# Kernel tuning notes

Measured on AMD Instinct MI355X. Metric: run time of the kernel, lower is better.

Reference implementation:

```python
import jax, jax.numpy as jnp
import numpy as np

B, S, H = 4, 2048, 768
NUM_HEADS = 12
HEAD_DIM = H // NUM_HEADS


def setup_inputs() -> dict:
    key = jax.random.key(0)
    k1, k2, k3 = jax.random.split(key, 3)
    hidden_states = jax.random.normal(k1, (B, S, H), dtype=jnp.float32)
    # torch Linear weight [out,in]; store transposed [in,out] for x @ W
    w_qkv = jax.random.normal(k2, (H, 3 * H), dtype=jnp.float32) * (1.0 / np.sqrt(H))
    w_out = jax.random.normal(k3, (H, H), dtype=jnp.float32) * (1.0 / np.sqrt(H))
    return {"hidden_states": hidden_states, "w_qkv": w_qkv, "w_out": w_out}


def reference(hidden_states, w_qkv, w_out):
    b, s, h = hidden_states.shape
    qkv = hidden_states @ w_qkv                      # [b,s,3h]
    qkv = qkv.reshape(b, s, 3, NUM_HEADS, HEAD_DIM)
    qkv = jnp.transpose(qkv, (2, 0, 3, 1, 4))        # [3,b,nh,s,hd]
    q, k, v = qkv[0], qkv[1], qkv[2]
    scale = 1.0 / np.sqrt(HEAD_DIM).astype(np.float32)
    scores = jnp.einsum('bhqd,bhkd->bhqk', q, k) * scale   # [b,nh,s,s]
    causal = jnp.triu(jnp.ones((s, s), dtype=bool), k=1)
    scores = jnp.where(causal, jnp.float32(-jnp.inf), scores)
    attn = jax.nn.softmax(scores, axis=-1)
    # dropout is identity in eval mode
    out = jnp.einsum('bhqk,bhkd->bhqd', attn, v)      # [b,nh,s,hd]
    out = jnp.transpose(out, (0, 2, 1, 3)).reshape(b, s, h)
    return out @ w_out
```

## Files before the change

### kernel.cpp

```cpp
#include <hip/hip_runtime.h>
#include <stdint.h>

#define B_ 4
#define S_ 2048
#define H_ 768
#define NH_ 12
#define HD_ 64
#define BH_ (B_ * NH_)

#define QSCALE 0.18033688011112042f

typedef __attribute__((ext_vector_type(4))) float f32x4;
typedef __attribute__((ext_vector_type(16))) float f32x16;
typedef __attribute__((ext_vector_type(8))) __bf16 bf16x8;
typedef __attribute__((ext_vector_type(8))) unsigned short ushort8;
typedef __attribute__((ext_vector_type(2))) unsigned int u32x2;
typedef __attribute__((ext_vector_type(4))) unsigned int u32x4;

__device__ __forceinline__ unsigned short bf16rne(float f) {
  union { float f; unsigned int u; } v;
  v.f = f;
  unsigned int u = v.u;
  return (unsigned short)((u + 0x7fffu + ((u >> 16) & 1u)) >> 16);
}

#if __has_builtin(__builtin_amdgcn_cvt_pk_bf16_f32)
__device__ __forceinline__ unsigned int pk2(float a, float b) {
  auto r = __builtin_amdgcn_cvt_pk_bf16_f32(a, b);
  return *(unsigned int*)&r;
}
#else
__device__ __forceinline__ unsigned int pk2(float a, float b) {
  return (unsigned int)bf16rne(a) | ((unsigned int)bf16rne(b) << 16);
}
#endif

#if __has_builtin(__builtin_amdgcn_exp2f)
#define EXP2F(x) __builtin_amdgcn_exp2f(x)
#else
#define EXP2F(x) exp2f(x)
#endif

#if __has_builtin(__builtin_amdgcn_permlane32_swap)
__device__ __forceinline__ u32x2 permswap(unsigned a, unsigned b) {
  u32x2 r = __builtin_amdgcn_permlane32_swap(a, b, false, false);
  return r;
}
#else
__device__ __forceinline__ u32x2 permswap(unsigned a, unsigned b) {
  int l = (int)(threadIdx.x & 63);
  unsigned ap = (unsigned)__shfl((int)a, l ^ 32, 64);
  unsigned bp = (unsigned)__shfl((int)b, l ^ 32, 64);
  u32x2 r;
  r[0] = (l & 32) ? bp : a;
  r[1] = (l & 32) ? b : ap;
  return r;
}
#endif

__device__ __forceinline__ void gll16(const void* g, void* l) {
  __builtin_amdgcn_global_load_lds(
      (const __attribute__((address_space(1))) unsigned int*)g,
      (__attribute__((address_space(3))) unsigned int*)l, 16, 0, 0);
}

__device__ __forceinline__ void tconv_body(const float* __restrict__ in,
                                           unsigned short* __restrict__ out,
                                           int R, int C, int bx, int by,
                                           unsigned short (*tile)[72], int tid) {
  int c0 = bx * 64, r0 = by * 64;
#pragma unroll
  for (int i = 0; i < 4; ++i) {
    int c = i * 256 + tid;
    int row = c >> 4, col4 = (c & 15) * 4;
    float4 v = *(const float4*)(in + (size_t)(r0 + row) * C + c0 + col4);
    *(uint2*)(&tile[row][col4]) = (uint2){pk2(v.x, v.y), pk2(v.z, v.w)};
  }
  __syncthreads();
#pragma unroll
  for (int i = 0; i < 2; ++i) {
    int c = i * 256 + tid;
    int oc = c >> 3, r8 = (c & 7) * 8;
    ushort8 v;
#pragma unroll
    for (int j = 0; j < 8; ++j) v[j] = tile[r8 + j][oc];
    *(ushort8*)(out + (size_t)(c0 + oc) * R + r0 + r8) = v;
  }
}

__global__ __launch_bounds__(256) void prep_kernel(const float* __restrict__ hs,
                                                   const float* __restrict__ wqkv,
                                                   const float* __restrict__ wout,
                                                   unsigned short* __restrict__ Xbf,
                                                   unsigned short* __restrict__ Wqkvt,
                                                   unsigned short* __restrict__ Woutt) {
  __shared__ unsigned short tile[64][72];
  int bid = blockIdx.x, tid = threadIdx.x;
  if (bid < 3072) {
    int i = (bid * 256 + tid) * 8;
    const float4* p = (const float4*)(hs + i);
    float4 a = p[0], b = p[1];
    uint4 r = {pk2(a.x, a.y), pk2(a.z, a.w), pk2(b.x, b.y), pk2(b.z, b.w)};
    *(uint4*)(Xbf + i) = r;
  } else if (bid < 3504) {
    int idx = bid - 3072;
    tconv_body(wqkv, Wqkvt, 768, 2304, idx % 36, idx / 36, tile, tid);
  } else {
    int idx = bid - 3504;
    tconv_body(wout, Woutt, 768, 768, idx % 12, idx / 12, tile, tid);
  }
}

template <int MODE>
__device__ __forceinline__ void gemm_core(const unsigned short* __restrict__ A,
                                          const unsigned short* __restrict__ Bm,
                                          void* __restrict__ Cout, int N, int K,
                                          int bm, int bn,
                                          unsigned short* As, unsigned short* Bs) {
  int tid = threadIdx.x;
  int lane = tid & 63, wave = tid >> 6;
  int quad = lane >> 4, l16 = lane & 15;
  int wm = (wave & 1) * 64, wn = (wave >> 1) * 64;
  const unsigned short* Ag = A + (size_t)bm * 128 * K;
  const unsigned short* Bg = Bm + (size_t)bn * 128 * K;

  f32x4 zero = {0.f, 0.f, 0.f, 0.f};
  f32x4 acc[4][4];
#pragma unroll
  for (int mt = 0; mt < 4; ++mt)
#pragma unroll
    for (int nt = 0; nt < 4; ++nt) acc[mt][nt] = zero;

  for (int k0 = 0; k0 < K; k0 += 32) {
#pragma unroll
    for (int i = 0; i < 2; ++i) {
      int c = i * 256 + tid;
      int row = c >> 2, off = (c & 3) * 8;
      gll16(Ag + (size_t)row * K + k0 + off, As + c * 8);
      gll16(Bg + (size_t)row * K + k0 + off, Bs + c * 8);
    }
    __syncthreads();
    bf16x8 af[4], bf[4];
#pragma unroll
    for (int mt = 0; mt < 4; ++mt)
      af[mt] = *(const bf16x8*)(As + (wm + mt * 16 + l16) * 32 + quad * 8);
#pragma unroll
    for (int nt = 0; nt < 4; ++nt)
      bf[nt] = *(const bf16x8*)(Bs + (wn + nt * 16 + l16) * 32 + quad * 8);
#pragma unroll
    for (int mt = 0; mt < 4; ++mt)
#pragma unroll
      for (int nt = 0; nt < 4; ++nt) {
        if (MODE == 2)
          acc[mt][nt] = __builtin_amdgcn_mfma_f32_16x16x32_bf16(af[mt], bf[nt], acc[mt][nt], 0, 0, 0);
        else
          acc[mt][nt] = __builtin_amdgcn_mfma_f32_16x16x32_bf16(bf[nt], af[mt], acc[mt][nt], 0, 0, 0);
      }
    __syncthreads();
  }

  if (MODE == 0) {
    unsigned short* qkv = (unsigned short*)Cout;
    int which = (bn >= 6);
#pragma unroll
    for (int mt = 0; mt < 4; ++mt)
#pragma unroll
      for (int nt = 0; nt < 4; ++nt) {
        int f0 = bn * 128 + wn + nt * 16 + quad * 4;
        int tm = bm * 128 + wm + mt * 16 + l16;
        int rem = f0 - which * 768;
        int head = rem >> 6, d0 = rem & 63;
        int b = tm >> 11, s = tm & 2047;
        if (which == 0) {
          uint2 pkv = {pk2(acc[mt][nt][0] * QSCALE, acc[mt][nt][1] * QSCALE),
                       pk2(acc[mt][nt][2] * QSCALE, acc[mt][nt][3] * QSCALE)};
          *(uint2*)(qkv + (((size_t)b * NH_ + head) * S_ + s) * HD_ + d0) = pkv;
        } else {
          uint2 pkv = {pk2(acc[mt][nt][0], acc[mt][nt][1]),
                       pk2(acc[mt][nt][2], acc[mt][nt][3])};
          int t = s >> 6, kb = (s >> 5) & 1, row = s & 31;
          int dk = d0 >> 4, hh = (d0 >> 3) & 1, off = d0 & 7;
          *(uint2*)(qkv + ((size_t)(BH_ + b * NH_ + head)) * S_ * HD_ + t * 4096
                    + ((kb * 4 + dk) * 64 + hh * 32 + row) * 8 + off) = pkv;
        }
      }
  } else {
    unsigned short* vt = (unsigned short*)Cout;
#pragma unroll
    for (int mt = 0; mt < 4; ++mt)
#pragma unroll
      for (int nt = 0; nt < 4; ++nt) {
        int f = bn * 128 + wn + nt * 16 + l16;
        int t0 = bm * 128 + wm + mt * 16 + quad * 4;
        int rem = f - 1536;
        int head = rem >> 6, d = rem & 63;
        int b = t0 >> 11, s0 = t0 & 2047;
        int tile = s0 >> 6, sin = s0 & 63;
        int ks = sin >> 4, hh = (sin >> 3) & 1, off = sin & 7;
        int db = d >> 5, drow = d & 31;
        uint2 pkv = {pk2(acc[mt][nt][0], acc[mt][nt][1]),
                     pk2(acc[mt][nt][2], acc[mt][nt][3])};
        *(uint2*)(vt + ((size_t)(b * NH_ + head)) * HD_ * S_ + tile * 4096
                  + ((db * 4 + ks) * 64 + hh * 32 + drow) * 8 + off) = pkv;
      }
  }
}

__global__ __launch_bounds__(256) void gemm_qkv(const unsigned short* __restrict__ A,
                                                const unsigned short* __restrict__ Bm,
                                                unsigned short* __restrict__ QK,
                                                unsigned short* __restrict__ Vt) {
  __shared__ unsigned short As[128 * 32];
  __shared__ unsigned short Bs[128 * 32];
  int bm = blockIdx.x, bn = blockIdx.y;
  if (bn < 12)
    gemm_core<0>(A, Bm, QK, 2304, 768, bm, bn, As, Bs);
  else
    gemm_core<2>(A, Bm, Vt, 2304, 768, bm, bn, As, Bs);
}

__global__ __launch_bounds__(256) void gemm_out64(const unsigned short* __restrict__ A,
                                                  const unsigned short* __restrict__ Bm,
                                                  float* __restrict__ Cout) {
  __shared__ unsigned short As[64 * 32];
  __shared__ unsigned short Bs[128 * 32];
  const int K = 768, N = 768;
  int bm = blockIdx.x, bn = blockIdx.y;
  int tid = threadIdx.x, lane = tid & 63, wave = tid >> 6;
  int quad = lane >> 4, l16 = lane & 15;
  int wn = wave * 32;
  const unsigned short* Ag = A + (size_t)bm * 64 * K;
  const unsigned short* Bg = Bm + (size_t)bn * 128 * K;

  f32x4 zero = {0.f, 0.f, 0.f, 0.f};
  f32x4 acc[4][2];
#pragma unroll
  for (int mt = 0; mt < 4; ++mt)
#pragma unroll
    for (int nt = 0; nt < 2; ++nt) acc[mt][nt] = zero;

  for (int k0 = 0; k0 < K; k0 += 32) {
    {
      int row = tid >> 2, off = (tid & 3) * 8;
      gll16(Ag + (size_t)row * K + k0 + off, As + tid * 8);
    }
#pragma unroll
    for (int i = 0; i < 2; ++i) {
      int c = i * 256 + tid;
      int row = c >> 2, off = (c & 3) * 8;
      gll16(Bg + (size_t)row * K + k0 + off, Bs + c * 8);
    }
    __syncthreads();
    bf16x8 af[4], bf[2];
#pragma unroll
    for (int mt = 0; mt < 4; ++mt)
      af[mt] = *(const bf16x8*)(As + (mt * 16 + l16) * 32 + quad * 8);
#pragma unroll
    for (int nt = 0; nt < 2; ++nt)
      bf[nt] = *(const bf16x8*)(Bs + (wn + nt * 16 + l16) * 32 + quad * 8);
#pragma unroll
    for (int mt = 0; mt < 4; ++mt)
#pragma unroll
      for (int nt = 0; nt < 2; ++nt)
        acc[mt][nt] = __builtin_amdgcn_mfma_f32_16x16x32_bf16(bf[nt], af[mt], acc[mt][nt], 0, 0, 0);
    __syncthreads();
  }

#pragma unroll
  for (int mt = 0; mt < 4; ++mt)
#pragma unroll
    for (int nt = 0; nt < 2; ++nt) {
      int f0 = bn * 128 + wn + nt * 16 + quad * 4;
      int tm = bm * 64 + mt * 16 + l16;
      *(f32x4*)(Cout + (size_t)tm * N + f0) = acc[mt][nt];
    }
}

__global__ __launch_bounds__(256, 4) void attn_kernel(const unsigned short* __restrict__ Q,
                                                      const unsigned short* __restrict__ Kg,
                                                      const unsigned short* __restrict__ Vt,
                                                      unsigned short* __restrict__ O) {
  __shared__ unsigned short Ks[2][64 * 64];
  __shared__ unsigned short Vs[2][64 * 64];
  const int pi_[16] = {0, 1, 3, 5, 7, 9, 11, 13, 15, 14, 12, 10, 8, 6, 4, 2};
  int bh = blockIdx.x;
  int y = blockIdx.y;
  int qt = pi_[(bh + y) & 15];
  int tid = threadIdx.x, lane = tid & 63, wave = tid >> 6;
  int l32 = lane & 31, h = lane >> 5;
  const unsigned short* Qp = Q + (size_t)bh * S_ * HD_;
  int q0 = qt * 128;
  int qrow = q0 + wave * 32 + l32;
  int kmax_w = (q0 + wave * 32 + 31) >> 6;
  int kmax_b = 2 * qt + 1;

  const unsigned short* kS = Kg + (size_t)bh * S_ * HD_;
  const unsigned short* vS = Vt + (size_t)bh * HD_ * S_;

  auto stage = [&](int t, int buf) {
#pragma unroll
    for (int i = 0; i < 2; ++i) {
      int c = (i * 256 + tid) * 8;
      gll16(kS + (size_t)t * 4096 + c, &Ks[buf][c]);
      gll16(vS + (size_t)t * 4096 + c, &Vs[buf][c]);
    }
  };

  stage(0, 0);

  bf16x8 qf[4];
#pragma unroll
  for (int dk = 0; dk < 4; ++dk)
    qf[dk] = *(const bf16x8*)(Qp + (size_t)qrow * HD_ + dk * 16 + h * 8);

  bf16x8 ones;
#pragma unroll
  for (int j = 0; j < 8; ++j) ones[j] = (__bf16)1.0f;

  const int flin = lane * 8;

  f32x16 zero16;
#pragma unroll
  for (int j = 0; j < 16; ++j) zero16[j] = 0.f;
  f32x16 o[2], rsv;
  o[0] = zero16; o[1] = zero16; rsv = zero16;

  auto body = [&](int t, const unsigned short* Kb, const unsigned short* Vb) {
    f32x16 sf[2];
    sf[0] = zero16; sf[1] = zero16;
    __builtin_amdgcn_s_setprio(1);
#pragma unroll
    for (int kb = 0; kb < 2; ++kb)
#pragma unroll
      for (int dk = 0; dk < 4; ++dk) {
        bf16x8 kf = *(const bf16x8*)(Kb + (kb * 4 + dk) * 512 + flin);
        sf[kb] = __builtin_amdgcn_mfma_f32_32x32x16_bf16(kf, qf[dk], sf[kb], 0, 0, 0);
      }
    __builtin_amdgcn_s_setprio(0);

    if (t == kmax_w) {
#pragma unroll
      for (int kb = 0; kb < 2; ++kb)
#pragma unroll
        for (int r = 0; r < 16; ++r)
          if (t * 64 + kb * 32 + (r & 3) + 8 * (r >> 2) + 4 * h > qrow) sf[kb][r] = -1e30f;
    }

    unsigned p01[8], p23[8];
#pragma unroll
    for (int kb = 0; kb < 2; ++kb)
#pragma unroll
      for (int g = 0; g < 4; ++g) {
        p01[kb * 4 + g] = pk2(EXP2F(sf[kb][g * 4 + 0]), EXP2F(sf[kb][g * 4 + 1]));
        p23[kb * 4 + g] = pk2(EXP2F(sf[kb][g * 4 + 2]), EXP2F(sf[kb][g * 4 + 3]));
      }

#pragma unroll
    for (int ks = 0; ks < 4; ++ks) {
      u32x2 a02 = permswap(p01[2 * ks], p01[2 * ks + 1]);
      u32x2 a13 = permswap(p23[2 * ks], p23[2 * ks + 1]);
      u32x4 pu;
      pu[0] = a02[0]; pu[1] = a13[0]; pu[2] = a02[1]; pu[3] = a13[1];
      bf16x8 pf = *(bf16x8*)&pu;
      __builtin_amdgcn_s_setprio(1);
      rsv = __builtin_amdgcn_mfma_f32_32x32x16_bf16(ones, pf, rsv, 0, 0, 0);
#pragma unroll
      for (int db = 0; db < 2; ++db) {
        bf16x8 vf = *(const bf16x8*)(Vb + (db * 4 + ks) * 512 + flin);
        o[db] = __builtin_amdgcn_mfma_f32_32x32x16_bf16(vf, pf, o[db], 0, 0, 0);
      }
      __builtin_amdgcn_s_setprio(0);
    }
  };

  for (int t = 0; t <= kmax_b; t += 2) {
    __syncthreads();
    stage(t + 1, 1);
    if (t <= kmax_w) body(t, &Ks[0][0], &Vs[0][0]);
    __syncthreads();
    if (t + 2 <= kmax_b) stage(t + 2, 0);
    if (t + 1 <= kmax_w) body(t + 1, &Ks[1][0], &Vs[1][0]);
  }

  float inv = 1.f / rsv[0];
  int b = bh / NH_, hh = bh % NH_;
#pragma unroll
  for (int db = 0; db < 2; ++db)
#pragma unroll
    for (int g = 0; g < 4; ++g) {
      uint2 pkv = {pk2(o[db][g * 4 + 0] * inv, o[db][g * 4 + 1] * inv),
                   pk2(o[db][g * 4 + 2] * inv, o[db][g * 4 + 3] * inv)};
      int d0 = db * 32 + 8 * g + 4 * h;
      *(uint2*)(O + ((size_t)b * S_ + qrow) * H_ + hh * HD_ + d0) = pkv;
    }
}

extern "C" void kernel_launch(void* const* d_in, const int* in_sizes, int n_in,
                              void* d_out, int out_size, void* d_ws, size_t ws_size,
                              hipStream_t stream) {
  (void)in_sizes; (void)n_in; (void)out_size; (void)ws_size;
  const float* hs = (const float*)d_in[0];
  const float* wqkv = (const float*)d_in[1];
  const float* wout = (const float*)d_in[2];
  float* out = (float*)d_out;

  unsigned short* Xbf = (unsigned short*)d_ws;
  unsigned short* Wqkvt = Xbf + (size_t)8192 * 768;
  unsigned short* Woutt = Wqkvt + (size_t)2304 * 768;
  unsigned short* QK = Woutt + (size_t)768 * 768;
  unsigned short* Vt = QK + (size_t)2 * BH_ * S_ * HD_;
  unsigned short* Attn = Xbf;

  prep_kernel<<<3648, 256, 0, stream>>>(hs, wqkv, wout, Xbf, Wqkvt, Woutt);
  gemm_qkv<<<dim3(64, 18), 256, 0, stream>>>(Xbf, Wqkvt, QK, Vt);
  attn_kernel<<<dim3(48, 16), 256, 0, stream>>>(QK, QK + (size_t)BH_ * S_ * HD_, Vt, Attn);
  gemm_out64<<<dim3(128, 6), 256, 0, stream>>>(Attn, Woutt, out);
}
```

Measured before the change: 195.3 us.

## Drop LDS staging in attention; pair complementary causal q-tiles per block

The attention kernel stops double-buffering K/V tiles through shared memory and instead reads them directly from global memory (relying on cache) inside each wave. Blocks shrink to two waves, each handling one 32-row query tile, paired as y and 63-y so that causal work is balanced. On the diagonal tile, half of the key block is skipped when it is fully masked. This removes the __syncthreads barriers and LDS traffic but gives up the shared-tile reuse across waves, so global/L2 load traffic goes up.

```diff
diff --git a/kernel.cpp b/kernel.cpp
--- a/kernel.cpp
+++ b/kernel.cpp
@@ -276,37 +276,23 @@
     }
 }
 
-__global__ __launch_bounds__(256, 4) void attn_kernel(const unsigned short* __restrict__ Q,
+__global__ __launch_bounds__(128, 3) void attn_kernel(const unsigned short* __restrict__ Q,
                                                       const unsigned short* __restrict__ Kg,
                                                       const unsigned short* __restrict__ Vt,
                                                       unsigned short* __restrict__ O) {
-  __shared__ unsigned short Ks[2][64 * 64];
-  __shared__ unsigned short Vs[2][64 * 64];
-  const int pi_[16] = {0, 1, 3, 5, 7, 9, 11, 13, 15, 14, 12, 10, 8, 6, 4, 2};
   int bh = blockIdx.x;
   int y = blockIdx.y;
-  int qt = pi_[(bh + y) & 15];
-  int tid = threadIdx.x, lane = tid & 63, wave = tid >> 6;
+  int tid = threadIdx.x, lane = tid & 63, w = tid >> 6;
   int l32 = lane & 31, h = lane >> 5;
+  int qt = w ? y : 63 - y;
+  int qrow = qt * 32 + l32;
+  int kmax = qt >> 1;
+  int diagodd = qt & 1;
+
   const unsigned short* Qp = Q + (size_t)bh * S_ * HD_;
-  int q0 = qt * 128;
-  int qrow = q0 + wave * 32 + l32;
-  int kmax_w = (q0 + wave * 32 + 31) >> 6;
-  int kmax_b = 2 * qt + 1;
-
-  const unsigned short* kS = Kg + (size_t)bh * S_ * HD_;
-  const unsigned short* vS = Vt + (size_t)bh * HD_ * S_;
-
-  auto stage = [&](int t, int buf) {
-#pragma unroll
-    for (int i = 0; i < 2; ++i) {
-      int c = (i * 256 + tid) * 8;
-      gll16(kS + (size_t)t * 4096 + c, &Ks[buf][c]);
-      gll16(vS + (size_t)t * 4096 + c, &Vs[buf][c]);
-    }
-  };
-
-  stage(0, 0);
+  const unsigned short* Kb0 = Kg + (size_t)bh * S_ * HD_;
+  const unsigned short* Vb0 = Vt + (size_t)bh * HD_ * S_;
+  const int flin = lane * 8;
 
   bf16x8 qf[4];
 #pragma unroll
@@ -316,8 +302,6 @@
   bf16x8 ones;
 #pragma unroll
   for (int j = 0; j < 8; ++j) ones[j] = (__bf16)1.0f;
-
-  const int flin = lane * 8;
 
   f32x16 zero16;
 #pragma unroll
@@ -325,61 +309,58 @@
   f32x16 o[2], rsv;
   o[0] = zero16; o[1] = zero16; rsv = zero16;
 
-  auto body = [&](int t, const unsigned short* Kb, const unsigned short* Vb) {
+  for (int t = 0; t <= kmax; ++t) {
+    const unsigned short* Kb = Kb0 + (size_t)t * 4096;
+    const unsigned short* Vb = Vb0 + (size_t)t * 4096;
+    int last = (t == kmax);
+    int nkb = (last && !diagodd) ? 1 : 2;
+
     f32x16 sf[2];
     sf[0] = zero16; sf[1] = zero16;
-    __builtin_amdgcn_s_setprio(1);
 #pragma unroll
     for (int kb = 0; kb < 2; ++kb)
-#pragma unroll
-      for (int dk = 0; dk < 4; ++dk) {
-        bf16x8 kf = *(const bf16x8*)(Kb + (kb * 4 + dk) * 512 + flin);
-        sf[kb] = __builtin_amdgcn_mfma_f32_32x32x16_bf16(kf, qf[dk], sf[kb], 0, 0, 0);
+      if (kb < nkb)
+#pragma unroll
+        for (int dk = 0; dk < 4; ++dk) {
+          bf16x8 kf = *(const bf16x8*)(Kb + (kb * 4 + dk) * 512 + flin);
+          sf[kb] = __builtin_amdgcn_mfma_f32_32x32x16_bf16(kf, qf[dk], sf[kb], 0, 0, 0);
+        }
+
+    if (last) {
+#pragma unroll
+      for (int kb = 0; kb < 2; ++kb)
+        if (kb < nkb)
+#pragma unroll
+          for (int r = 0; r < 16; ++r)
+            if (t * 64 + kb * 32 + (r & 3) + 8 * (r >> 2) + 4 * h > qrow) sf[kb][r] = -1e30f;
+    }
+
+    unsigned p01[8], p23[8];
+#pragma unroll
+    for (int kb = 0; kb < 2; ++kb)
+      if (kb < nkb)
+#pragma unroll
+        for (int g = 0; g < 4; ++g) {
+          p01[kb * 4 + g] = pk2(EXP2F(sf[kb][g * 4 + 0]), EXP2F(sf[kb][g * 4 + 1]));
+          p23[kb * 4 + g] = pk2(EXP2F(sf[kb][g * 4 + 2]), EXP2F(sf[kb][g * 4 + 3]));
+        }
+
+    int nks = nkb * 2;
+#pragma unroll
+    for (int ks = 0; ks < 4; ++ks)
+      if (ks < nks) {
+        u32x2 a02 = permswap(p01[2 * ks], p01[2 * ks + 1]);
+        u32x2 a13 = permswap(p23[2 * ks], p23[2 * ks + 1]);
+        u32x4 pu;
+        pu[0] = a02[0]; pu[1] = a13[0]; pu[2] = a02[1]; pu[3] = a13[1];
+        bf16x8 pf = *(bf16x8*)&pu;
+        rsv = __builtin_amdgcn_mfma_f32_32x32x16_bf16(ones, pf, rsv, 0, 0, 0);
+#pragma unroll
+        for (int db = 0; db < 2; ++db) {
+          bf16x8 vf = *(const bf16x8*)(Vb + (db * 4 + ks) * 512 + flin);
+          o[db] = __builtin_amdgcn_mfma_f32_32x32x16_bf16(vf, pf, o[db], 0, 0, 0);
+        }
       }
-    __builtin_amdgcn_s_setprio(0);
-
-    if (t == kmax_w) {
-#pragma unroll
-      for (int kb = 0; kb < 2; ++kb)
-#pragma unroll
-        for (int r = 0; r < 16; ++r)
-          if (t * 64 + kb * 32 + (r & 3) + 8 * (r >> 2) + 4 * h > qrow) sf[kb][r] = -1e30f;
-    }
-
-    unsigned p01[8], p23[8];
-#pragma unroll
-    for (int kb = 0; kb < 2; ++kb)
-#pragma unroll
-      for (int g = 0; g < 4; ++g) {
-        p01[kb * 4 + g] = pk2(EXP2F(sf[kb][g * 4 + 0]), EXP2F(sf[kb][g * 4 + 1]));
-        p23[kb * 4 + g] = pk2(EXP2F(sf[kb][g * 4 + 2]), EXP2F(sf[kb][g * 4 + 3]));
-      }
-
-#pragma unroll
-    for (int ks = 0; ks < 4; ++ks) {
-      u32x2 a02 = permswap(p01[2 * ks], p01[2 * ks + 1]);
-      u32x2 a13 = permswap(p23[2 * ks], p23[2 * ks + 1]);
-      u32x4 pu;
-      pu[0] = a02[0]; pu[1] = a13[0]; pu[2] = a02[1]; pu[3] = a13[1];
-      bf16x8 pf = *(bf16x8*)&pu;
-      __builtin_amdgcn_s_setprio(1);
-      rsv = __builtin_amdgcn_mfma_f32_32x32x16_bf16(ones, pf, rsv, 0, 0, 0);
-#pragma unroll
-      for (int db = 0; db < 2; ++db) {
-        bf16x8 vf = *(const bf16x8*)(Vb + (db * 4 + ks) * 512 + flin);
-        o[db] = __builtin_amdgcn_mfma_f32_32x32x16_bf16(vf, pf, o[db], 0, 0, 0);
-      }
-      __builtin_amdgcn_s_setprio(0);
-    }
-  };
-
-  for (int t = 0; t <= kmax_b; t += 2) {
-    __syncthreads();
-    stage(t + 1, 1);
-    if (t <= kmax_w) body(t, &Ks[0][0], &Vs[0][0]);
-    __syncthreads();
-    if (t + 2 <= kmax_b) stage(t + 2, 0);
-    if (t + 1 <= kmax_w) body(t + 1, &Ks[1][0], &Vs[1][0]);
   }
 
   float inv = 1.f / rsv[0];
@@ -413,6 +394,6 @@
 
   prep_kernel<<<3648, 256, 0, stream>>>(hs, wqkv, wout, Xbf, Wqkvt, Woutt);
   gemm_qkv<<<dim3(64, 18), 256, 0, stream>>>(Xbf, Wqkvt, QK, Vt);
-  attn_kernel<<<dim3(48, 16), 256, 0, stream>>>(QK, QK + (size_t)BH_ * S_ * HD_, Vt, Attn);
+  attn_kernel<<<dim3(48, 32), 128, 0, stream>>>(QK, QK + (size_t)BH_ * S_ * HD_, Vt, Attn);
   gemm_out64<<<dim3(128, 6), 256, 0, stream>>>(Attn, Woutt, out);
 }
```

After: 238.5 us. +22.1%, slower.
